# Kernel tuning notes

Measured on AMD Instinct MI355X. Metric: run time of the kernel, lower is better.

Reference implementation:

```python
import jax, jax.numpy as jnp
import numpy as np

B, S, HID = 2, 2048, 1024
H, D = 16, 64
KD = H * D
RMS_EPS = 1e-5
L2_EPS = 1e-12


def setup_inputs() -> dict:
    key = jax.random.key(0)
    ks = jax.random.split(key, 9)
    w = lambda k, shape: jax.random.normal(k, shape, jnp.float32) * 0.02
    return {
        "x": jax.random.normal(ks[0], (B, S, HID), jnp.float32),
        "Wq": w(ks[1], (HID, KD)),
        "Wk": w(ks[2], (HID, KD)),
        "Wv": w(ks[3], (HID, KD)),
        "Wf": w(ks[4], (HID, KD)),
        "Wb": w(ks[5], (HID, H)),
        "A_log": jnp.log(jnp.full((H,), 8.0, jnp.float32)),
        "dt_bias": jnp.zeros((KD,), jnp.float32),
        "Wg": w(ks[6], (HID, KD)),
        "bg": jnp.zeros((KD,), jnp.float32),
        "Wo": w(ks[7], (KD, HID)),
        "norm_w": jnp.ones((D,), jnp.float32),
    }


def _l2norm(t):
    n = jnp.sqrt(jnp.sum(t * t, axis=-1, keepdims=True))
    return t / jnp.clip(n, L2_EPS)


def reference(x, Wq, Wk, Wv, Wf, Wb, A_log, dt_bias, Wg, bg, Wo, norm_w):
    b, s, _ = x.shape
    h = A_log.shape[0]
    d = norm_w.shape[0]

    q = jax.nn.silu(x @ Wq).reshape(b, s, h, d)
    k = jax.nn.silu(x @ Wk).reshape(b, s, h, d)
    v = jax.nn.silu(x @ Wv).reshape(b, s, h, d)
    g = (x @ Wf).reshape(b, s, h, d)
    beta = jax.nn.sigmoid(x @ Wb)  # [b,s,h]

    q = _l2norm(q)
    k = _l2norm(k)
    g = jax.nn.sigmoid(g - dt_bias.reshape(h, d))
    A = jnp.exp(-jnp.exp(A_log))  # [h]

    # seq-major for scan: [s, b, h, d]
    qs = jnp.moveaxis(q, 1, 0)
    kss = jnp.moveaxis(k, 1, 0)
    vs = jnp.moveaxis(v, 1, 0)
    gs = jnp.moveaxis(g, 1, 0)
    bs = jnp.moveaxis(beta, 1, 0)  # [s,b,h]

    state0 = jnp.zeros((b, h, d, d), x.dtype)

    def step(state, inp):
        q_t, k_t, v_t, g_t, b_t = inp
        o_t = jnp.einsum('bhd,bhde->bhe', q_t, state) * g_t
        state = A[None, :, None, None] * state \
            + b_t[..., None, None] * (k_t[..., :, None] * v_t[..., None, :])
        return state, o_t

    _, o = jax.lax.scan(step, state0, (qs, kss, vs, gs, bs))
    o = jnp.moveaxis(o, 0, 1)  # [b,s,h,d]

    # RMSNorm over head_dim, then gate
    o = o * jax.lax.rsqrt(jnp.mean(o * o, axis=-1, keepdims=True) + RMS_EPS) * norm_w
    gate = jax.nn.sigmoid(x @ Wg + bg).reshape(b, s, h, d)
    o = (o * gate).reshape(b, s, h * d)
    return o @ Wo
```

## Files before the change

kernel.cpp:

```cpp
#include <hip/hip_runtime.h>
#include <hip/hip_bf16.h>

typedef __hip_bfloat16 bf16;
typedef __attribute__((ext_vector_type(8))) short v8s;
typedef __attribute__((ext_vector_type(4))) short v4s;
typedef __attribute__((ext_vector_type(4))) float v4f;

#define MFMA16(a,b,c) __builtin_amdgcn_mfma_f32_16x16x32_bf16((a),(b),(c),0,0,0)
#define SCHED0() __builtin_amdgcn_sched_barrier(0)


static const size_t OFF_XBF    = 0;
static const size_t OFF_WCATT  = 8388608;
static const size_t OFF_WOT    = OFF_WCATT + 11010048;
static const size_t OFF_Y      = OFF_WOT + 2097152;
static const size_t OFF_BETA   = OFF_Y + 41943040;
static const size_t OFF_OPRE   = OFF_XBF;

__device__ __forceinline__ void gl2lds16(const bf16* g, bf16* l) {
  __builtin_amdgcn_global_load_lds(
      (const __attribute__((address_space(1))) void*)g,
      (__attribute__((address_space(3))) void*)l, 16, 0, 0);
}

__global__ __launch_bounds__(256) void cvt_x(const float* __restrict__ x, bf16* __restrict__ xb) {
  int t = blockIdx.x * 256 + threadIdx.x;
  int row = t >> 7, ch = t & 127;
  const float* src = x + (size_t)row * 1024 + ch * 8;
  v4f v0 = *(const v4f*)src;
  v4f v1 = *(const v4f*)(src + 4);
  union { bf16 h[8]; v8s s; } u;
  for (int i = 0; i < 4; ++i) { u.h[i] = __float2bfloat16(v0[i]); u.h[4+i] = __float2bfloat16(v1[i]); }
  int ch2 = (ch & ~3) | ((ch ^ (row >> 1)) & 3);
  *(v8s*)(xb + (size_t)row * 1024 + ch2 * 8) = u.s;
}

__global__ __launch_bounds__(256) void transpose_pack(
    const float* __restrict__ W0, const float* __restrict__ W1, const float* __restrict__ W2,
    const float* __restrict__ W3, const float* __restrict__ W4, const float* __restrict__ W5,
    bf16* __restrict__ WcatT, bf16* __restrict__ WoT)
{
  int mi = blockIdx.z;
  const float* W = (mi==0)?W0:(mi==1)?W1:(mi==2)?W2:(mi==3)?W3:(mi==4)?W4:W5;
  bf16* out = (mi < 5) ? (WcatT + (size_t)mi * 1048576) : WoT;
  __shared__ float tile[64][65];
  int c0 = blockIdx.x * 64;
  int r0 = blockIdx.y * 64;
  int l = threadIdx.x & 63, w = threadIdx.x >> 6;
  for (int i = 0; i < 16; ++i)
    tile[w + 4*i][l] = W[(size_t)(r0 + w + 4*i) * 1024 + c0 + l];
  __syncthreads();
  for (int i = 0; i < 16; ++i) {
    int orow = c0 + w + 4*i;
    int q = l >> 3;
    int q2 = (mi < 5) ? ((q & ~3) | ((q ^ (orow >> 1)) & 3))
                      : ((q ^ orow) & 7);
    int col = r0 + (q2 << 3) + (l & 7);
    out[(size_t)orow * 1024 + col] = __float2bfloat16(tile[l][w + 4*i]);
  }
}

__global__ __launch_bounds__(128) void pack_wb(const float* __restrict__ Wb, bf16* __restrict__ out) {
  int j = blockIdx.x;
  int ch = threadIdx.x;
  union { bf16 h[8]; v8s s; } u;
  for (int i = 0; i < 8; ++i)
    u.h[i] = __float2bfloat16(j < 16 ? Wb[(size_t)(ch*8 + i) * 16 + j] : 0.f);
  int row = 5120 + j;
  int ch2 = (ch & ~3) | ((ch ^ (row >> 1)) & 3);
  *(v8s*)(out + (size_t)j * 1024 + ch2 * 8) = u.s;
}

__global__ __launch_bounds__(256, 2) void gemm_main(
    const bf16* __restrict__ A, const bf16* __restrict__ BT,
    bf16* __restrict__ Yb, const float* __restrict__ dtb,
    const float* __restrict__ bgp, float* __restrict__ betaOut)
{
  __shared__ bf16 As[2][4096];
  __shared__ bf16 Bs[2][8192];
  const int tid = threadIdx.x;
  const int xcd = (int)blockIdx.x & 7, p = (int)blockIdx.x >> 3;
  const int by = xcd * 4 + (p & 3);
  const int bx = p >> 2;
  const int m0 = by * 128, n0 = bx * 256;
  const int w = tid >> 6, l = tid & 63;
  const int wr = w >> 1, wc = w & 1;
  const int lr = l & 15, lkq = l >> 4;
  const int cq = ((lkq ^ ((lr >> 1) & 3)) << 3);
  const int arow0 = (wr * 64 + lr) * 32;
  const int brow0 = (wc * 128 + lr) * 32;

  v4f acc[4][8];
  #pragma unroll
  for (int i = 0; i < 4; ++i)
    #pragma unroll
    for (int j = 0; j < 8; ++j) acc[i][j] = (v4f){0.f,0.f,0.f,0.f};

#define STG(t_, buf_) do { \
  gl2lds16(&A[(size_t)(m0 + (tid >> 2)) * 1024 + (t_)*32 + (tid & 3)*8], \
           &As[buf_][tid*8]); \
  gl2lds16(&A[(size_t)(m0 + 64 + (tid >> 2)) * 1024 + (t_)*32 + (tid & 3)*8], \
           &As[buf_][2048 + tid*8]); \
  gl2lds16(&BT[(size_t)(n0 + (tid >> 2)) * 1024 + (t_)*32 + (tid & 3)*8], \
           &Bs[buf_][tid*8]); \
  gl2lds16(&BT[(size_t)(n0 + 64 + (tid >> 2)) * 1024 + (t_)*32 + (tid & 3)*8], \
           &Bs[buf_][2048 + tid*8]); \
  gl2lds16(&BT[(size_t)(n0 + 128 + (tid >> 2)) * 1024 + (t_)*32 + (tid & 3)*8], \
           &Bs[buf_][4096 + tid*8]); \
  gl2lds16(&BT[(size_t)(n0 + 192 + (tid >> 2)) * 1024 + (t_)*32 + (tid & 3)*8], \
           &Bs[buf_][6144 + tid*8]); \
} while(0)

  STG(0, 0); SCHED0();
  STG(1, 1); SCHED0();

  for (int t = 0; t < 32; ++t) {
    const int cur = t & 1;
    if (t == 31) { asm volatile("s_waitcnt vmcnt(0)" ::: "memory"); }
    else         { asm volatile("s_waitcnt vmcnt(6)" ::: "memory"); }
    SCHED0();
    __builtin_amdgcn_s_barrier();
    SCHED0();
    const bf16* Ab = &As[cur][0];
    const bf16* Bb = &Bs[cur][0];
    v8s afr[4], bfr[8];
    #pragma unroll
    for (int mt = 0; mt < 4; ++mt)
      afr[mt] = *(const v8s*)(Ab + arow0 + mt*512 + cq);
    #pragma unroll
    for (int nt = 0; nt < 8; ++nt)
      bfr[nt] = *(const v8s*)(Bb + brow0 + nt*512 + cq);
    asm volatile("s_waitcnt lgkmcnt(0)" ::: "memory");
    SCHED0();
    __builtin_amdgcn_s_barrier();
    SCHED0();
    if (t + 2 < 32) { STG(t + 2, cur); }
    __builtin_amdgcn_s_setprio(1);
    #pragma unroll
    for (int mt = 0; mt < 4; ++mt)
      #pragma unroll
      for (int nt = 0; nt < 8; ++nt)
        acc[mt][nt] = MFMA16(afr[mt], bfr[nt], acc[mt][nt]);
    __builtin_amdgcn_s_setprio(0);
  }
#undef STG

  const int region = (n0 + wc * 128) >> 10;
  #pragma unroll
  for (int mt = 0; mt < 4; ++mt)
    #pragma unroll
    for (int r = 0; r < 4; ++r) {
      int gm = m0 + wr * 64 + mt * 16 + lkq * 4 + r;
      float v[8];
      if (region < 2) {
        #pragma unroll
        for (int hh = 0; hh < 2; ++hh) {
          float ss = 0.f;
          #pragma unroll
          for (int q4 = 0; q4 < 4; ++q4) {
            float y = acc[mt][hh*4 + q4][r];
            float s = y / (1.f + __expf(-y));
            v[hh*4 + q4] = s; ss += s * s;
          }
          ss += __shfl_xor(ss, 1, 64); ss += __shfl_xor(ss, 2, 64);
          ss += __shfl_xor(ss, 4, 64); ss += __shfl_xor(ss, 8, 64);
          float inv = 1.f / fmaxf(sqrtf(ss), 1e-12f);
          #pragma unroll
          for (int q4 = 0; q4 < 4; ++q4) v[hh*4 + q4] *= inv;
        }
      } else if (region == 2) {
        #pragma unroll
        for (int nt = 0; nt < 8; ++nt) {
          float y = acc[mt][nt][r];
          v[nt] = y / (1.f + __expf(-y));
        }
      } else if (region == 3) {
        #pragma unroll
        for (int nt = 0; nt < 8; ++nt) {
          int gn = n0 + wc * 128 + nt * 16 + lr;
          float z = acc[mt][nt][r] - dtb[gn & 1023];
          v[nt] = 1.f / (1.f + __expf(-z));
        }
      } else if (region == 4) {
        #pragma unroll
        for (int nt = 0; nt < 8; ++nt) {
          int gn = n0 + wc * 128 + nt * 16 + lr;
          float z = acc[mt][nt][r] + bgp[gn & 1023];
          v[nt] = 1.f / (1.f + __expf(-z));
        }
      } else {
        #pragma unroll
        for (int nt = 0; nt < 8; ++nt) {
          int gn = n0 + wc * 128 + nt * 16 + lr;
          if (gn < 5136)
            betaOut[(size_t)gm * 16 + (gn - 5120)] =
                1.f / (1.f + __expf(-acc[mt][nt][r]));
        }
        continue;
      }
      #pragma unroll
      for (int nt = 0; nt < 8; ++nt) {
        int gn = n0 + wc * 128 + nt * 16 + lr;
        Yb[(size_t)gm * 5120 + gn] = __float2bfloat16(v[nt]);
      }
    }
}

__global__ __launch_bounds__(256) void gemm_out(
    const bf16* __restrict__ A, const bf16* __restrict__ BT,
    float* __restrict__ Co)
{
  __shared__ bf16 As[2][8192];
  __shared__ bf16 Bs[2][8192];
  const int tid = threadIdx.x;
  int swzb = ((int)blockIdx.x & 7) * 32 + ((int)blockIdx.x >> 3);
  const int by = swzb >> 3, bx = swzb & 7;
  const int m0 = by * 128, n0 = bx * 128;
  const int w = tid >> 6, l = tid & 63;
  const int wm = (w >> 1) * 64, wn = (w & 1) * 64;
  const int lr = l & 15, lkq = l >> 4;
  const int xorv = lr & 7;
  const int c0 = ((lkq ^ xorv) << 3), c1 = (((4 + lkq) ^ xorv) << 3);
  v4f acc[4][4];
  for (int i = 0; i < 4; ++i) for (int j = 0; j < 4; ++j) acc[i][j] = (v4f){0.f,0.f,0.f,0.f};

#define STAGE(kk, buf) \
  for (int i_ = 0; i_ < 4; ++i_) { \
    int eo_ = (i_ * 256 + tid) * 8; \
    int r_ = eo_ >> 6, cc_ = eo_ & 63; \
    gl2lds16(&A[(size_t)(m0 + r_) * 1024 + (kk) + cc_], &As[buf][eo_]); \
    gl2lds16(&BT[(size_t)(n0 + r_) * 1024 + (kk) + cc_], &Bs[buf][eo_]); \
  }

  STAGE(0, 0);
  __syncthreads();
  int cur = 0;
  for (int kk = 0; kk < 1024; kk += 64) {
    if (kk + 64 < 1024) { STAGE(kk + 64, cur ^ 1); }
    v8s af[2][4], bfr[2][4];
    #pragma unroll
    for (int mt = 0; mt < 4; ++mt) {
      af[0][mt] = *(const v8s*)(&As[cur][(wm + mt*16 + lr) * 64 + c0]);
      af[1][mt] = *(const v8s*)(&As[cur][(wm + mt*16 + lr) * 64 + c1]);
      bfr[0][mt] = *(const v8s*)(&Bs[cur][(wn + mt*16 + lr) * 64 + c0]);
      bfr[1][mt] = *(const v8s*)(&Bs[cur][(wn + mt*16 + lr) * 64 + c1]);
    }
    #pragma unroll
    for (int kc = 0; kc < 2; ++kc)
      #pragma unroll
      for (int mt = 0; mt < 4; ++mt)
        #pragma unroll
        for (int nt = 0; nt < 4; ++nt)
          acc[mt][nt] = MFMA16(af[kc][mt], bfr[kc][nt], acc[mt][nt]);
    __syncthreads();
    cur ^= 1;
  }
#undef STAGE
  #pragma unroll
  for (int mt = 0; mt < 4; ++mt)
    #pragma unroll
    for (int nt = 0; nt < 4; ++nt)
      #pragma unroll
      for (int r = 0; r < 4; ++r) {
        int gm = m0 + wm + mt*16 + lkq*4 + r;
        int gn = n0 + wn + nt*16 + lr;
        Co[(size_t)gm * 1024 + gn] = acc[mt][nt][r];
      }
}

__global__ __launch_bounds__(256) void passFused(
    const bf16* __restrict__ Y, const float* __restrict__ beta,
    const float* __restrict__ A_log, const float* __restrict__ norm_w,
    bf16* __restrict__ opre)
{
  int c = blockIdx.x, bh = blockIdx.y;
  int b = bh >> 4, h = bh & 15;
  int row0 = b * 2048 + c * 64;
  int prow0 = row0 - 64;
  bool hasPrev = (c > 0);
  __shared__ bf16 Qs[64][72], Ks[64][72], Vt[64][72];
  __shared__ bf16 Kp[64][72], Vp[64][72];
  __shared__ bf16 Ps[64][72], St[64][72];
  __shared__ float betas[64], pw[64];
  int tid = threadIdx.x, w = tid >> 6, l = tid & 63;
  float aexp = __expf(A_log[h]);
  if (tid < 64) {
    pw[tid] = __expf(-aexp * (float)tid);
    betas[tid] = beta[(size_t)(row0 + tid) * 16 + h];
  }
  __syncthreads();
  for (int i = 0; i < 2; ++i) {
    int cid = i * 256 + tid;
    int r = cid >> 3, c8 = (cid & 7) * 8;
    size_t ybase = (size_t)(row0 + r) * 5120 + h * 64 + c8;
    v8s q8 = *(const v8s*)(&Y[ybase]);
    v8s k8 = *(const v8s*)(&Y[ybase + 1024]);
    v8s v8 = *(const v8s*)(&Y[ybase + 2048]);
    *(v8s*)(&Qs[r][c8]) = q8;
    *(v8s*)(&Ks[r][c8]) = k8;
    const bf16* vpt = (const bf16*)&v8;
    for (int jj = 0; jj < 8; ++jj) Vt[c8 + jj][r] = vpt[jj];
    if (hasPrev) {
      size_t pbase = (size_t)(prow0 + r) * 5120 + h * 64 + c8;
      v8s pk8 = *(const v8s*)(&Y[pbase + 1024]);
      v8s pv8 = *(const v8s*)(&Y[pbase + 2048]);
      float coefT = pw[63 - r] * beta[(size_t)(prow0 + r) * 16 + h];
      const bf16* pkp = (const bf16*)&pk8;
      const bf16* pvp = (const bf16*)&pv8;
      for (int jj = 0; jj < 8; ++jj) {
        Kp[c8 + jj][r] = __float2bfloat16(coefT * __bfloat162float(pkp[jj]));
        Vp[c8 + jj][r] = pvp[jj];
      }
    } else {
      bf16 z = __float2bfloat16(0.f);
      for (int jj = 0; jj < 8; ++jj) { Kp[c8 + jj][r] = z; Vp[c8 + jj][r] = z; }
    }
  }
  __syncthreads();
  const int lr = l & 15, lk = (l >> 4) * 8;
  v4f accT[4], accP[4];
  for (int nt = 0; nt < 4; ++nt) { accT[nt] = (v4f){0.f,0.f,0.f,0.f}; accP[nt] = (v4f){0.f,0.f,0.f,0.f}; }
  for (int kc = 0; kc < 2; ++kc) {
    v8s av = *(const v8s*)(&Vp[w*16 + lr][kc*32 + lk]);
    v8s aq = *(const v8s*)(&Qs[w*16 + lr][kc*32 + lk]);
    for (int nt = 0; nt < 4; ++nt) {
      v8s bk = *(const v8s*)(&Kp[nt*16 + lr][kc*32 + lk]);
      v8s bc = *(const v8s*)(&Ks[nt*16 + lr][kc*32 + lk]);
      accT[nt] = MFMA16(av, bk, accT[nt]);
      accP[nt] = MFMA16(aq, bc, accP[nt]);
    }
  }
  for (int nt = 0; nt < 4; ++nt)
    for (int r = 0; r < 4; ++r) {
      int row = w*16 + (l>>4)*4 + r;
      int col = nt*16 + lr;
      St[row][col] = __float2bfloat16(accT[nt][r]);
      float v = accP[nt][r];
      float pm = (col < row) ? v * betas[col] * pw[row - 1 - col] : 0.f;
      Ps[row][col] = __float2bfloat16(pm);
    }
  __syncthreads();
  v4f accO[4], accI[4];
  for (int nt = 0; nt < 4; ++nt) { accO[nt] = (v4f){0.f,0.f,0.f,0.f}; accI[nt] = (v4f){0.f,0.f,0.f,0.f}; }
  for (int kc = 0; kc < 2; ++kc) {
    v8s ap = *(const v8s*)(&Ps[w*16 + lr][kc*32 + lk]);
    v8s aq = *(const v8s*)(&Qs[w*16 + lr][kc*32 + lk]);
    for (int nt = 0; nt < 4; ++nt) {
      v8s bv = *(const v8s*)(&Vt[nt*16 + lr][kc*32 + lk]);
      v8s bs = *(const v8s*)(&St[nt*16 + lr][kc*32 + lk]);
      accO[nt] = MFMA16(ap, bv, accO[nt]);
      accI[nt] = MFMA16(aq, bs, accI[nt]);
    }
  }
  for (int r = 0; r < 4; ++r) {
    int tq = w*16 + (l>>4)*4 + r;
    float sc = pw[tq];
    size_t orow = (size_t)(row0 + tq);
    float o[4];
    float ss = 0.f;
    for (int nt = 0; nt < 4; ++nt) {
      int e = nt*16 + lr;
      float v = accO[nt][r] + sc * accI[nt][r];
      float g = __bfloat162float(Y[orow * 5120 + 3072 + h*64 + e]);
      v *= g;
      o[nt] = v;
      ss += v * v;
    }
    ss += __shfl_xor(ss, 1, 64);
    ss += __shfl_xor(ss, 2, 64);
    ss += __shfl_xor(ss, 4, 64);
    ss += __shfl_xor(ss, 8, 64);
    float rms = rsqrtf(ss * (1.f/64.f) + 1e-5f);
    for (int nt = 0; nt < 4; ++nt) {
      int e = nt*16 + lr;
      float gate = __bfloat162float(Y[orow * 5120 + 4096 + h*64 + e]);
      float outv = o[nt] * rms * norm_w[e] * gate;
      int col = h*64 + ((((e >> 3)) ^ ((int)orow & 7)) << 3) + (e & 7);
      opre[orow * 1024 + col] = __float2bfloat16(outv);
    }
  }
}

extern "C" void kernel_launch(void* const* d_in, const int* in_sizes, int n_in,
                              void* d_out, int out_size, void* d_ws, size_t ws_size,
                              hipStream_t stream) {
  const float* x       = (const float*)d_in[0];
  const float* Wq      = (const float*)d_in[1];
  const float* Wk      = (const float*)d_in[2];
  const float* Wv      = (const float*)d_in[3];
  const float* Wf      = (const float*)d_in[4];
  const float* Wb      = (const float*)d_in[5];
  const float* A_log   = (const float*)d_in[6];
  const float* dt_bias = (const float*)d_in[7];
  const float* Wg      = (const float*)d_in[8];
  const float* bg      = (const float*)d_in[9];
  const float* Wo      = (const float*)d_in[10];
  const float* norm_w  = (const float*)d_in[11];

  char* ws = (char*)d_ws;
  bf16*  xb     = (bf16*)(ws + OFF_XBF);
  bf16*  wcatT  = (bf16*)(ws + OFF_WCATT);
  bf16*  woT    = (bf16*)(ws + OFF_WOT);
  bf16*  Y      = (bf16*)(ws + OFF_Y);
  float* beta   = (float*)(ws + OFF_BETA);
  bf16*  opre   = (bf16*)(ws + OFF_OPRE);

  cvt_x<<<2048, 256, 0, stream>>>(x, xb);
  transpose_pack<<<dim3(16, 16, 6), 256, 0, stream>>>(Wq, Wk, Wv, Wf, Wg, Wo, wcatT, woT);
  pack_wb<<<256, 128, 0, stream>>>(Wb, wcatT + (size_t)5120 * 1024);
  gemm_main<<<672, 256, 0, stream>>>(xb, wcatT, Y, dt_bias, bg, beta);
  passFused<<<dim3(32, 32), 256, 0, stream>>>(Y, beta, A_log, norm_w, opre);
  gemm_out<<<256, 256, 0, stream>>>(opre, woT, (float*)d_out);
}
```

Measured before the change: 138.1 us.

## Merge prep kernels into one launch and widen gemm_main to 512 threads

Merges the x conversion, weight transpose/pack and Wb pack kernels into one prep launch, removing two kernel launches and their gaps. gemm_main now runs 8 waves per block in a 2x4 layout, each wave computing a 64x64 tile instead of 64x128, with each thread issuing half as many global-to-LDS loads. This lowers per-thread accumulator registers and adds latency hiding, but means more LDS fragment reads per MFMA and more barrier participants. The L2-norm epilogue now reduces one 64-wide head per wave row.

```diff
diff --git a/kernel.cpp b/kernel.cpp
--- a/kernel.cpp
+++ b/kernel.cpp
@@ -23,55 +23,59 @@
       (__attribute__((address_space(3))) void*)l, 16, 0, 0);
 }
 
-__global__ __launch_bounds__(256) void cvt_x(const float* __restrict__ x, bf16* __restrict__ xb) {
-  int t = blockIdx.x * 256 + threadIdx.x;
-  int row = t >> 7, ch = t & 127;
-  const float* src = x + (size_t)row * 1024 + ch * 8;
-  v4f v0 = *(const v4f*)src;
-  v4f v1 = *(const v4f*)(src + 4);
-  union { bf16 h[8]; v8s s; } u;
-  for (int i = 0; i < 4; ++i) { u.h[i] = __float2bfloat16(v0[i]); u.h[4+i] = __float2bfloat16(v1[i]); }
-  int ch2 = (ch & ~3) | ((ch ^ (row >> 1)) & 3);
-  *(v8s*)(xb + (size_t)row * 1024 + ch2 * 8) = u.s;
-}
-
-__global__ __launch_bounds__(256) void transpose_pack(
-    const float* __restrict__ W0, const float* __restrict__ W1, const float* __restrict__ W2,
-    const float* __restrict__ W3, const float* __restrict__ W4, const float* __restrict__ W5,
-    bf16* __restrict__ WcatT, bf16* __restrict__ WoT)
+__global__ __launch_bounds__(256) void prep(
+    const float* __restrict__ x,
+    const float* __restrict__ W0, const float* __restrict__ W1,
+    const float* __restrict__ W2, const float* __restrict__ W3,
+    const float* __restrict__ W4, const float* __restrict__ W5,
+    const float* __restrict__ Wb,
+    bf16* __restrict__ xb, bf16* __restrict__ WcatT, bf16* __restrict__ WoT)
 {
-  int mi = blockIdx.z;
-  const float* W = (mi==0)?W0:(mi==1)?W1:(mi==2)?W2:(mi==3)?W3:(mi==4)?W4:W5;
-  bf16* out = (mi < 5) ? (WcatT + (size_t)mi * 1048576) : WoT;
   __shared__ float tile[64][65];
-  int c0 = blockIdx.x * 64;
-  int r0 = blockIdx.y * 64;
-  int l = threadIdx.x & 63, w = threadIdx.x >> 6;
-  for (int i = 0; i < 16; ++i)
-    tile[w + 4*i][l] = W[(size_t)(r0 + w + 4*i) * 1024 + c0 + l];
-  __syncthreads();
-  for (int i = 0; i < 16; ++i) {
-    int orow = c0 + w + 4*i;
-    int q = l >> 3;
-    int q2 = (mi < 5) ? ((q & ~3) | ((q ^ (orow >> 1)) & 3))
-                      : ((q ^ orow) & 7);
-    int col = r0 + (q2 << 3) + (l & 7);
-    out[(size_t)orow * 1024 + col] = __float2bfloat16(tile[l][w + 4*i]);
-  }
-}
-
-__global__ __launch_bounds__(128) void pack_wb(const float* __restrict__ Wb, bf16* __restrict__ out) {
-  int j = blockIdx.x;
-  int ch = threadIdx.x;
-  union { bf16 h[8]; v8s s; } u;
-  for (int i = 0; i < 8; ++i)
-    u.h[i] = __float2bfloat16(j < 16 ? Wb[(size_t)(ch*8 + i) * 16 + j] : 0.f);
-  int row = 5120 + j;
-  int ch2 = (ch & ~3) | ((ch ^ (row >> 1)) & 3);
-  *(v8s*)(out + (size_t)j * 1024 + ch2 * 8) = u.s;
-}
-
-__global__ __launch_bounds__(256, 2) void gemm_main(
+  int bid = blockIdx.x;
+  if (bid < 2048) {
+    int t = bid * 256 + threadIdx.x;
+    int row = t >> 7, ch = t & 127;
+    const float* src = x + (size_t)row * 1024 + ch * 8;
+    v4f v0 = *(const v4f*)src;
+    v4f v1 = *(const v4f*)(src + 4);
+    union { bf16 h[8]; v8s s; } u;
+    for (int i = 0; i < 4; ++i) { u.h[i] = __float2bfloat16(v0[i]); u.h[4+i] = __float2bfloat16(v1[i]); }
+    int ch2 = (ch & ~3) | ((ch ^ (row >> 1)) & 3);
+    *(v8s*)(xb + (size_t)row * 1024 + ch2 * 8) = u.s;
+  } else if (bid < 3584) {
+    int b2 = bid - 2048;
+    int mi = b2 >> 8;
+    int rem = b2 & 255;
+    int c0 = (rem & 15) * 64;
+    int r0 = (rem >> 4) * 64;
+    const float* W = (mi==0)?W0:(mi==1)?W1:(mi==2)?W2:(mi==3)?W3:(mi==4)?W4:W5;
+    bf16* out = (mi < 5) ? (WcatT + (size_t)mi * 1048576) : WoT;
+    int l = threadIdx.x & 63, w = threadIdx.x >> 6;
+    for (int i = 0; i < 16; ++i)
+      tile[w + 4*i][l] = W[(size_t)(r0 + w + 4*i) * 1024 + c0 + l];
+    __syncthreads();
+    for (int i = 0; i < 16; ++i) {
+      int orow = c0 + w + 4*i;
+      int q = l >> 3;
+      int q2 = (mi < 5) ? ((q & ~3) | ((q ^ (orow >> 1)) & 3))
+                        : ((q ^ orow) & 7);
+      int col = r0 + (q2 << 3) + (l & 7);
+      out[(size_t)orow * 1024 + col] = __float2bfloat16(tile[l][w + 4*i]);
+    }
+  } else {
+    int j = (bid - 3584) * 2 + (threadIdx.x >> 7);
+    int ch = threadIdx.x & 127;
+    union { bf16 h[8]; v8s s; } u;
+    for (int i = 0; i < 8; ++i)
+      u.h[i] = __float2bfloat16(j < 16 ? Wb[(size_t)(ch*8 + i) * 16 + j] : 0.f);
+    int row = 5120 + j;
+    int ch2 = (ch & ~3) | ((ch ^ (row >> 1)) & 3);
+    *(v8s*)(WcatT + (size_t)row * 1024 + ch2 * 8) = u.s;
+  }
+}
+
+__global__ __launch_bounds__(512, 2) void gemm_main(
     const bf16* __restrict__ A, const bf16* __restrict__ BT,
     bf16* __restrict__ Yb, const float* __restrict__ dtb,
     const float* __restrict__ bgp, float* __restrict__ betaOut)
@@ -84,31 +88,25 @@
   const int bx = p >> 2;
   const int m0 = by * 128, n0 = bx * 256;
   const int w = tid >> 6, l = tid & 63;
-  const int wr = w >> 1, wc = w & 1;
+  const int wr = w >> 2, wc = w & 3;
   const int lr = l & 15, lkq = l >> 4;
   const int cq = ((lkq ^ ((lr >> 1) & 3)) << 3);
   const int arow0 = (wr * 64 + lr) * 32;
-  const int brow0 = (wc * 128 + lr) * 32;
-
-  v4f acc[4][8];
+  const int brow0 = (wc * 64 + lr) * 32;
+
+  v4f acc[4][4];
   #pragma unroll
   for (int i = 0; i < 4; ++i)
     #pragma unroll
-    for (int j = 0; j < 8; ++j) acc[i][j] = (v4f){0.f,0.f,0.f,0.f};
+    for (int j = 0; j < 4; ++j) acc[i][j] = (v4f){0.f,0.f,0.f,0.f};
 
 #define STG(t_, buf_) do { \
   gl2lds16(&A[(size_t)(m0 + (tid >> 2)) * 1024 + (t_)*32 + (tid & 3)*8], \
            &As[buf_][tid*8]); \
-  gl2lds16(&A[(size_t)(m0 + 64 + (tid >> 2)) * 1024 + (t_)*32 + (tid & 3)*8], \
-           &As[buf_][2048 + tid*8]); \
   gl2lds16(&BT[(size_t)(n0 + (tid >> 2)) * 1024 + (t_)*32 + (tid & 3)*8], \
            &Bs[buf_][tid*8]); \
-  gl2lds16(&BT[(size_t)(n0 + 64 + (tid >> 2)) * 1024 + (t_)*32 + (tid & 3)*8], \
-           &Bs[buf_][2048 + tid*8]); \
   gl2lds16(&BT[(size_t)(n0 + 128 + (tid >> 2)) * 1024 + (t_)*32 + (tid & 3)*8], \
            &Bs[buf_][4096 + tid*8]); \
-  gl2lds16(&BT[(size_t)(n0 + 192 + (tid >> 2)) * 1024 + (t_)*32 + (tid & 3)*8], \
-           &Bs[buf_][6144 + tid*8]); \
 } while(0)
 
   STG(0, 0); SCHED0();
@@ -117,18 +115,18 @@
   for (int t = 0; t < 32; ++t) {
     const int cur = t & 1;
     if (t == 31) { asm volatile("s_waitcnt vmcnt(0)" ::: "memory"); }
-    else         { asm volatile("s_waitcnt vmcnt(6)" ::: "memory"); }
+    else         { asm volatile("s_waitcnt vmcnt(3)" ::: "memory"); }
     SCHED0();
     __builtin_amdgcn_s_barrier();
     SCHED0();
     const bf16* Ab = &As[cur][0];
     const bf16* Bb = &Bs[cur][0];
-    v8s afr[4], bfr[8];
+    v8s afr[4], bfr[4];
     #pragma unroll
     for (int mt = 0; mt < 4; ++mt)
       afr[mt] = *(const v8s*)(Ab + arow0 + mt*512 + cq);
     #pragma unroll
-    for (int nt = 0; nt < 8; ++nt)
+    for (int nt = 0; nt < 4; ++nt)
       bfr[nt] = *(const v8s*)(Bb + brow0 + nt*512 + cq);
     asm volatile("s_waitcnt lgkmcnt(0)" ::: "memory");
     SCHED0();
@@ -139,59 +137,56 @@
     #pragma unroll
     for (int mt = 0; mt < 4; ++mt)
       #pragma unroll
-      for (int nt = 0; nt < 8; ++nt)
+      for (int nt = 0; nt < 4; ++nt)
         acc[mt][nt] = MFMA16(afr[mt], bfr[nt], acc[mt][nt]);
     __builtin_amdgcn_s_setprio(0);
   }
 #undef STG
 
-  const int region = (n0 + wc * 128) >> 10;
+  const int region = (n0 + wc * 64) >> 10;
   #pragma unroll
   for (int mt = 0; mt < 4; ++mt)
     #pragma unroll
     for (int r = 0; r < 4; ++r) {
       int gm = m0 + wr * 64 + mt * 16 + lkq * 4 + r;
-      float v[8];
+      float v[4];
       if (region < 2) {
-        #pragma unroll
-        for (int hh = 0; hh < 2; ++hh) {
-          float ss = 0.f;
-          #pragma unroll
-          for (int q4 = 0; q4 < 4; ++q4) {
-            float y = acc[mt][hh*4 + q4][r];
-            float s = y / (1.f + __expf(-y));
-            v[hh*4 + q4] = s; ss += s * s;
-          }
-          ss += __shfl_xor(ss, 1, 64); ss += __shfl_xor(ss, 2, 64);
-          ss += __shfl_xor(ss, 4, 64); ss += __shfl_xor(ss, 8, 64);
-          float inv = 1.f / fmaxf(sqrtf(ss), 1e-12f);
-          #pragma unroll
-          for (int q4 = 0; q4 < 4; ++q4) v[hh*4 + q4] *= inv;
+        float ss = 0.f;
+        #pragma unroll
+        for (int nt = 0; nt < 4; ++nt) {
+          float y = acc[mt][nt][r];
+          float s = y / (1.f + __expf(-y));
+          v[nt] = s; ss += s * s;
         }
+        ss += __shfl_xor(ss, 1, 64); ss += __shfl_xor(ss, 2, 64);
+        ss += __shfl_xor(ss, 4, 64); ss += __shfl_xor(ss, 8, 64);
+        float inv = 1.f / fmaxf(sqrtf(ss), 1e-12f);
+        #pragma unroll
+        for (int nt = 0; nt < 4; ++nt) v[nt] *= inv;
       } else if (region == 2) {
         #pragma unroll
-        for (int nt = 0; nt < 8; ++nt) {
+        for (int nt = 0; nt < 4; ++nt) {
           float y = acc[mt][nt][r];
           v[nt] = y / (1.f + __expf(-y));
         }
       } else if (region == 3) {
         #pragma unroll
-        for (int nt = 0; nt < 8; ++nt) {
-          int gn = n0 + wc * 128 + nt * 16 + lr;
+        for (int nt = 0; nt < 4; ++nt) {
+          int gn = n0 + wc * 64 + nt * 16 + lr;
           float z = acc[mt][nt][r] - dtb[gn & 1023];
           v[nt] = 1.f / (1.f + __expf(-z));
         }
       } else if (region == 4) {
         #pragma unroll
-        for (int nt = 0; nt < 8; ++nt) {
-          int gn = n0 + wc * 128 + nt * 16 + lr;
+        for (int nt = 0; nt < 4; ++nt) {
+          int gn = n0 + wc * 64 + nt * 16 + lr;
           float z = acc[mt][nt][r] + bgp[gn & 1023];
           v[nt] = 1.f / (1.f + __expf(-z));
         }
       } else {
         #pragma unroll
-        for (int nt = 0; nt < 8; ++nt) {
-          int gn = n0 + wc * 128 + nt * 16 + lr;
+        for (int nt = 0; nt < 4; ++nt) {
+          int gn = n0 + wc * 64 + nt * 16 + lr;
           if (gn < 5136)
             betaOut[(size_t)gm * 16 + (gn - 5120)] =
                 1.f / (1.f + __expf(-acc[mt][nt][r]));
@@ -199,8 +194,8 @@
         continue;
       }
       #pragma unroll
-      for (int nt = 0; nt < 8; ++nt) {
-        int gn = n0 + wc * 128 + nt * 16 + lr;
+      for (int nt = 0; nt < 4; ++nt) {
+        int gn = n0 + wc * 64 + nt * 16 + lr;
         Yb[(size_t)gm * 5120 + gn] = __float2bfloat16(v[nt]);
       }
     }
@@ -405,10 +400,8 @@
   float* beta   = (float*)(ws + OFF_BETA);
   bf16*  opre   = (bf16*)(ws + OFF_OPRE);
 
-  cvt_x<<<2048, 256, 0, stream>>>(x, xb);
-  transpose_pack<<<dim3(16, 16, 6), 256, 0, stream>>>(Wq, Wk, Wv, Wf, Wg, Wo, wcatT, woT);
-  pack_wb<<<256, 128, 0, stream>>>(Wb, wcatT + (size_t)5120 * 1024);
-  gemm_main<<<672, 256, 0, stream>>>(xb, wcatT, Y, dt_bias, bg, beta);
+  prep<<<3712, 256, 0, stream>>>(x, Wq, Wk, Wv, Wf, Wg, Wo, Wb, xb, wcatT, woT);
+  gemm_main<<<672, 512, 0, stream>>>(xb, wcatT, Y, dt_bias, bg, beta);
   passFused<<<dim3(32, 32), 256, 0, stream>>>(Y, beta, A_log, norm_w, opre);
   gemm_out<<<256, 256, 0, stream>>>(opre, woT, (float*)d_out);
 }
```

Result: faster. 135.2 us (-2.1%).
